# Performance work log

Measured on AMD Instinct MI355X. Metric: run time of the kernel, lower is better.

The kernel has to match this reference:

```python
import jax, jax.numpy as jnp
import numpy as np

BN_EPS = 1e-5

@jax.custom_vjp
def ste_sign(x):
    return jnp.sign(x)

def _ste_fwd(x):
    return jnp.sign(x), x

def _ste_bwd(x, g):
    # straight-through estimator with hardtanh clipping
    return (g * (jnp.abs(x) <= 1.0).astype(g.dtype),)

ste_sign.defvjp(_ste_fwd, _ste_bwd)

def bi_conv_bn_relu(h, W, scale, gamma, beta):
    # h: [B, Cin, K, N]; W: [Cout, Cin] (1x1 conv); scale/gamma/beta: [Cout]
    ba = ste_sign(h)                      # binarize activations
    bw = ste_sign(W)                      # binarize weights
    y = jnp.einsum('oi,bikn->bokn', bw, ba) * scale[None, :, None, None]
    # BatchNorm2d, training-mode batch statistics over (B, K, N)
    mean = jnp.mean(y, axis=(0, 2, 3), keepdims=True)
    var = jnp.var(y, axis=(0, 2, 3), keepdims=True)
    y = gamma[None, :, None, None] * (y - mean) * jax.lax.rsqrt(var + BN_EPS) + beta[None, :, None, None]
    return jax.nn.relu(y)

def setup_inputs() -> dict:
    key = jax.random.key(0)
    sizes = [64, 64, 64, 128]
    B, N, K = 8, 1024, 32
    ks = jax.random.split(key, 16)
    inp = {"agg_feat": jax.random.normal(ks[0], (B * N, K, sizes[0]), dtype=jnp.float32)}
    j = 1
    for i in range(1, len(sizes)):
        cin, cout = sizes[i - 1], sizes[i]
        inp[f"W{i}"] = jax.random.normal(ks[j], (cout, cin), dtype=jnp.float32) * 0.1; j += 1
        inp[f"s{i}"] = jax.random.uniform(ks[j], (cout,), dtype=jnp.float32, minval=0.05, maxval=0.2); j += 1
        inp[f"g{i}"] = jnp.ones((cout,), dtype=jnp.float32)
        inp[f"b{i}"] = jnp.zeros((cout,), dtype=jnp.float32)
    return inp

def reference(agg_feat, W1, s1, g1, b1, W2, s2, g2, b2, W3, s3, g3, b3):
    B = 8
    M, K, D = agg_feat.shape
    # view(B, -1, K, D).permute(0, 3, 2, 1) -> [B, D, K, N]
    h = agg_feat.reshape(B, M // B, K, D).transpose(0, 3, 2, 1)
    h = bi_conv_bn_relu(h, W1, s1, g1, b1)
    h = bi_conv_bn_relu(h, W2, s2, g2, b2)
    h = bi_conv_bn_relu(h, W3, s3, g3, b3)
    h = jnp.max(h, axis=2)                 # max-pool over neighbors -> [B, C, N]
    C = h.shape[1]
    return h.transpose(0, 2, 1).reshape(-1, C)  # [B*N, C]
```

## Files before the change

### kernel.cpp

```cpp
#include <hip/hip_runtime.h>


typedef unsigned long long u64;

#define P_TOTAL (8192 * 32)
#define NREP 16

__device__ __forceinline__ u64 bcast64(u64 x, int p) {
    unsigned lo = __builtin_amdgcn_readlane((unsigned)x, p);
    unsigned hi = __builtin_amdgcn_readlane((unsigned)(x >> 32), p);
    return ((u64)hi << 32) | lo;
}

__device__ __forceinline__ u64 pack_stats(int sd, int sq) {
    return ((u64)(unsigned)sd << 32) | (u64)(unsigned)sq;
}

__device__ __forceinline__ void affine_from_stats(const u64* __restrict__ st,
        int c, const float* __restrict__ scale, const float* __restrict__ gamma,
        const float* __restrict__ beta, int cparam, float& a, float& b) {
    u64 v = 0;
    #pragma unroll
    for (int r = 0; r < NREP; ++r) v += st[r * 256 + c];
    int sd = (int)(v >> 32);
    int sq = (int)(unsigned)(v & 0xFFFFFFFFull);
    const double invN = 1.0 / (double)P_TOTAL;
    double m = (double)sd * invN;
    double var = (double)sq * invN - m * m;
    double sc = (double)scale[cparam];
    double inv = 1.0 / sqrt(sc * sc * var + 1e-5);
    double g = (double)gamma[cparam];
    a = (float)(g * inv * sc);
    b = (float)((double)beta[cparam] - g * inv * sc * m);
}

__device__ __forceinline__ int make_thresh(float a, float b, bool& flip) {
    if (a == 0.f) { flip = false; return (b > 0.f) ? -65 : 65; }
    double r = -(double)b / (double)a;
    r = fmin(fmax(r, -1e6), 1e6);
    int t0 = (int)floor(r);
    int T;
    if (a > 0.f) {
        flip = false;
        T = t0 + 2;
        if (fmaf(a, (float)(t0 + 1), b) > 0.f) T = t0 + 1;
        if (fmaf(a, (float)(t0    ), b) > 0.f) T = t0;
        if (fmaf(a, (float)(t0 - 1), b) > 0.f) T = t0 - 1;
    } else {
        flip = true;
        int H = t0 - 2;
        if (fmaf(a, (float)(t0 - 1), b) > 0.f) H = t0 - 1;
        if (fmaf(a, (float)(t0    ), b) > 0.f) H = t0;
        if (fmaf(a, (float)(t0 + 1), b) > 0.f) H = t0 + 1;
        T = -H;
    }
    return max(-65, min(65, T));
}

__global__ void k0_pack(const float* __restrict__ W1, const float* __restrict__ W2,
                        const float* __restrict__ W3,
                        ulonglong2* __restrict__ wp1, ulonglong2* __restrict__ wp2,
                        ulonglong2* __restrict__ wp3, u64* __restrict__ stats) {
    int t = threadIdx.x;
    #pragma unroll
    for (int r = 0; r < NREP; ++r) stats[r * 256 + t] = 0;
    if (t < 64) {
        u64 s = 0, nz = 0;
        for (int c = 0; c < 64; ++c) {
            float w = W1[t * 64 + c];
            int p = ((c & 3) << 4) | (c >> 2);
            if (w > 0.f) s |= 1ull << p;
            if (w != 0.f) nz |= 1ull << p;
        }
        wp1[t] = make_ulonglong2(s, nz);
    } else if (t < 128) {
        int o = t - 64;
        u64 pos = 0, neg = 0;
        for (int c = 0; c < 64; ++c) {
            float w = W2[o * 64 + c];
            if (w > 0.f) pos |= 1ull << c;
            if (w < 0.f) neg |= 1ull << c;
        }
        wp2[o] = make_ulonglong2(pos, neg);
    } else {
        int o = t - 128;
        u64 pos = 0, neg = 0;
        for (int c = 0; c < 64; ++c) {
            float w = W3[o * 64 + c];
            if (w > 0.f) pos |= 1ull << c;
            if (w < 0.f) neg |= 1ull << c;
        }
        wp3[o] = make_ulonglong2(pos, neg);
    }
}

__global__ void __launch_bounds__(256) k1_pack_stats(
    const float4* __restrict__ in4, const ulonglong2* __restrict__ wp1,
    ulonglong2* __restrict__ A1, u64* __restrict__ stats) {
    const int lane = threadIdx.x & 63;
    const int wib = threadIdx.x >> 6;
    const int wid = (blockIdx.x << 2) | wib;
    const ulonglong2 w = wp1[lane];
    const int sh = (lane >> 4) << 4;
    const size_t base = (size_t)wid * 512 + lane;

    float4 v0 = in4[base];
    float4 v1 = in4[base + 64];
    float4 v2 = in4[base + 128];
    float4 v3 = in4[base + 192];
    float4 v4 = in4[base + 256];
    float4 v5 = in4[base + 320];
    float4 v6 = in4[base + 384];
    float4 v7 = in4[base + 448];

    int sd = 0, sq = 0;
    auto proc = [&](float4 v, int q0) {
        u64 bs0 = __ballot(v.x > 0.f), bn0 = __ballot(v.x != 0.f);
        u64 bs1 = __ballot(v.y > 0.f), bn1 = __ballot(v.y != 0.f);
        u64 bs2 = __ballot(v.z > 0.f), bn2 = __ballot(v.z != 0.f);
        u64 bs3 = __ballot(v.w > 0.f), bn3 = __ballot(v.w != 0.f);
        u64 myS = ((bs0 >> sh) & 0xFFFFull) | (((bs1 >> sh) & 0xFFFFull) << 16)
                | (((bs2 >> sh) & 0xFFFFull) << 32) | (((bs3 >> sh) & 0xFFFFull) << 48);
        u64 myN = ((bn0 >> sh) & 0xFFFFull) | (((bn1 >> sh) & 0xFFFFull) << 16)
                | (((bn2 >> sh) & 0xFFFFull) << 32) | (((bn3 >> sh) & 0xFFFFull) << 48);
        if ((lane & 15) == 0) A1[q0 + (lane >> 4)] = make_ulonglong2(myS, myN);
        #pragma unroll
        for (int p = 0; p < 4; ++p) {
            const int s2 = p << 4;
            u64 as = ((bs0 >> s2) & 0xFFFFull) | (((bs1 >> s2) & 0xFFFFull) << 16)
                   | (((bs2 >> s2) & 0xFFFFull) << 32) | (((bs3 >> s2) & 0xFFFFull) << 48);
            u64 an = ((bn0 >> s2) & 0xFFFFull) | (((bn1 >> s2) & 0xFFFFull) << 16)
                   | (((bn2 >> s2) & 0xFFFFull) << 32) | (((bn3 >> s2) & 0xFFFFull) << 48);
            u64 mnz = an & w.y;
            int dot = __popcll(mnz) - 2 * __popcll(mnz & (as ^ w.x));
            sd += dot; sq += dot * dot;
        }
    };
    const int q_base = wid * 32;
    proc(v0, q_base);      proc(v1, q_base + 4);
    proc(v2, q_base + 8);  proc(v3, q_base + 12);
    proc(v4, q_base + 16); proc(v5, q_base + 20);
    proc(v6, q_base + 24); proc(v7, q_base + 28);

    __shared__ int rd[4][64], rq[4][64];
    rd[wib][lane] = sd; rq[wib][lane] = sq;
    __syncthreads();
    if (threadIdx.x < 64) {
        int td = rd[0][lane] + rd[1][lane] + rd[2][lane] + rd[3][lane];
        int tq = rq[0][lane] + rq[1][lane] + rq[2][lane] + rq[3][lane];
        atomicAdd(&stats[(blockIdx.x & (NREP - 1)) * 256 + lane], pack_stats(td, tq));
    }
}

__global__ void __launch_bounds__(256, 4) k2_bin1_stats2(
    const ulonglong2* __restrict__ A1, const ulonglong2* __restrict__ wp1,
    const ulonglong2* __restrict__ wp2, const float* __restrict__ scale,
    const float* __restrict__ gamma, const float* __restrict__ beta,
    u64* __restrict__ A2, u64* __restrict__ stats) {
    const int lane = threadIdx.x & 63;
    const int wib = threadIdx.x >> 6;
    const int wid = (blockIdx.x << 2) | wib;
    float a, b;
    affine_from_stats(stats, lane, scale, gamma, beta, lane, a, b);
    bool flip;
    const int T = make_thresh(a, b, flip);
    ulonglong2 w1 = wp1[lane];
    const u64 w1S = flip ? ~w1.x : w1.x;
    const u64 w1N = w1.y;
    const ulonglong2 w2 = wp2[lane];

    const int q0 = wid * 64;
    const ulonglong2 aa = A1[q0 + lane];
    u64 mymask = 0;
    int sd = 0, sq = 0;
    #pragma unroll 8
    for (int p = 0; p < 64; ++p) {
        u64 as = bcast64(aa.x, p);
        u64 an = bcast64(aa.y, p);
        u64 mnz = an & w1N;
        int dot1 = __popcll(mnz) - 2 * __popcll(mnz & (as ^ w1S));
        u64 A = __ballot(dot1 >= T);
        mymask = (lane == p) ? A : mymask;
        int d2 = __popcll(A & w2.x) - __popcll(A & w2.y);
        sd += d2; sq += d2 * d2;
    }
    A2[q0 + lane] = mymask;

    __shared__ int rd[4][64], rq[4][64];
    rd[wib][lane] = sd; rq[wib][lane] = sq;
    __syncthreads();
    if (threadIdx.x < 64) {
        int td = rd[0][lane] + rd[1][lane] + rd[2][lane] + rd[3][lane];
        int tq = rq[0][lane] + rq[1][lane] + rq[2][lane] + rq[3][lane];
        atomicAdd(&stats[(blockIdx.x & (NREP - 1)) * 256 + 64 + lane], pack_stats(td, tq));
    }
}

__global__ void __launch_bounds__(256, 4) k3_bin2_stats3(
    const u64* __restrict__ A2, const ulonglong2* __restrict__ wp2,
    const ulonglong2* __restrict__ wp3, const float* __restrict__ scale,
    const float* __restrict__ gamma, const float* __restrict__ beta,
    short* __restrict__ dmm, u64* __restrict__ stats) {
    const int lane = threadIdx.x & 63;
    const int wib = threadIdx.x >> 6;
    const int wid = (blockIdx.x << 2) | wib;
    float a, b;
    affine_from_stats(stats, 64 + lane, scale, gamma, beta, lane, a, b);
    bool flip;
    const int T = make_thresh(a, b, flip);
    const ulonglong2 w2 = wp2[lane];
    const u64 w2P = flip ? w2.y : w2.x;
    const u64 w2N = flip ? w2.x : w2.y;
    const ulonglong2 w3a = wp3[lane];
    const ulonglong2 w3b = wp3[lane + 64];

    const int q0 = wid * 64;
    const u64 aa = A2[q0 + lane];
    int sda = 0, sqa = 0, sdb = 0, sqb = 0;
    #pragma unroll
    for (int r = 0; r < 2; ++r) {
        int maxa = -127, mina = 127, maxb = -127, minb = 127;
        #pragma unroll 8
        for (int pp = 0; pp < 32; ++pp) {
            const int p = (r << 5) | pp;
            u64 A = bcast64(aa, p);
            int d2 = __popcll(A & w2P) - __popcll(A & w2N);
            u64 A3 = __ballot(d2 >= T);
            int da = __popcll(A3 & w3a.x) - __popcll(A3 & w3a.y);
            int db = __popcll(A3 & w3b.x) - __popcll(A3 & w3b.y);
            sda += da; sqa += da * da; sdb += db; sqb += db * db;
            maxa = max(maxa, da); mina = min(mina, da);
            maxb = max(maxb, db); minb = min(minb, db);
        }
        const int m = (q0 >> 5) + r;
        dmm[m * 128 + lane]      = (short)((maxa & 0xFF) | ((mina & 0xFF) << 8));
        dmm[m * 128 + 64 + lane] = (short)((maxb & 0xFF) | ((minb & 0xFF) << 8));
    }
    __shared__ int rda[4][64], rqa[4][64], rdb[4][64], rqb[4][64];
    rda[wib][lane] = sda; rqa[wib][lane] = sqa;
    rdb[wib][lane] = sdb; rqb[wib][lane] = sqb;
    __syncthreads();
    if (threadIdx.x < 64) {
        const int rep = (blockIdx.x & (NREP - 1)) * 256;
        int tda = rda[0][lane] + rda[1][lane] + rda[2][lane] + rda[3][lane];
        int tqa = rqa[0][lane] + rqa[1][lane] + rqa[2][lane] + rqa[3][lane];
        int tdb = rdb[0][lane] + rdb[1][lane] + rdb[2][lane] + rdb[3][lane];
        int tqb = rqb[0][lane] + rqb[1][lane] + rqb[2][lane] + rqb[3][lane];
        atomicAdd(&stats[rep + 128 + lane], pack_stats(tda, tqa));
        atomicAdd(&stats[rep + 192 + lane], pack_stats(tdb, tqb));
    }
}

__global__ void __launch_bounds__(256) k4_out(
    const short* __restrict__ dmm, const float* __restrict__ scale,
    const float* __restrict__ gamma, const float* __restrict__ beta,
    const u64* __restrict__ stats, float* __restrict__ out) {
    __shared__ float sa[128], sb[128];
    if (threadIdx.x < 128)
        affine_from_stats(stats, 128 + threadIdx.x, scale, gamma, beta,
                          threadIdx.x, sa[threadIdx.x], sb[threadIdx.x]);
    __syncthreads();
    const int idx = blockIdx.x * 256 + threadIdx.x;
    const int o = idx & 127;
    short pk = dmm[idx];
    int mx = (signed char)(pk & 0xFF);
    int mn = (signed char)((pk >> 8) & 0xFF);
    float a = sa[o], b = sb[o];
    float v = fmaf(a, (float)(a >= 0.f ? mx : mn), b);
    out[idx] = fmaxf(v, 0.f);
}

extern "C" void kernel_launch(void* const* d_in, const int* in_sizes, int n_in,
                              void* d_out, int out_size, void* d_ws, size_t ws_size,
                              hipStream_t stream) {
    const float* agg = (const float*)d_in[0];
    const float* W1 = (const float*)d_in[1];
    const float* s1 = (const float*)d_in[2];
    const float* g1 = (const float*)d_in[3];
    const float* b1 = (const float*)d_in[4];
    const float* W2 = (const float*)d_in[5];
    const float* s2 = (const float*)d_in[6];
    const float* g2 = (const float*)d_in[7];
    const float* b2 = (const float*)d_in[8];
    const float* W3 = (const float*)d_in[9];
    const float* s3 = (const float*)d_in[10];
    const float* g3 = (const float*)d_in[11];
    const float* b3 = (const float*)d_in[12];
    float* out = (float*)d_out;

    char* ws = (char*)d_ws;
    ulonglong2* wp1 = (ulonglong2*)(ws + 0);
    ulonglong2* wp2 = (ulonglong2*)(ws + 1024);
    ulonglong2* wp3 = (ulonglong2*)(ws + 2048);
    u64* stats = (u64*)(ws + 4096);
    ulonglong2* A1 = (ulonglong2*)(ws + 65536);
    u64* A2 = (u64*)(ws + 65536 + (size_t)P_TOTAL * 16);
    short* dmm = (short*)(ws + 65536 + (size_t)P_TOTAL * 24);

    k0_pack<<<1, 256, 0, stream>>>(W1, W2, W3, wp1, wp2, wp3, stats);
    k1_pack_stats<<<2048, 256, 0, stream>>>((const float4*)agg, wp1, A1, stats);
    k2_bin1_stats2<<<1024, 256, 0, stream>>>(A1, wp1, wp2, s1, g1, b1, A2, stats);
    k3_bin2_stats3<<<1024, 256, 0, stream>>>(A2, wp2, wp3, s2, g2, b2, dmm, stats);
    k4_out<<<4096, 256, 0, stream>>>(dmm, s3, g3, b3, stats, out);
}
```

Before: 74.30 us.

## Halve per-wave work in bin kernels, share thresholds per block, vectorize weight pack

The binarized layer-2 and layer-3 kernels now have each wave handle 32 points instead of 64, with twice as many blocks launched, which doubles parallelism and shortens the serial readlane/ballot loop. Thresholds derived from batch statistics are computed once per block by 64 threads and shared through LDS, instead of being recomputed by every wave. The weight-packing kernel reads rows with float4 loads, and the output kernel uses 512-thread blocks. The occupancy hint in launch_bounds is dropped, and the extra block-level synchronization and doubled atomic traffic on the stats slots add some overhead.

```diff
diff --git a/kernel.cpp b/kernel.cpp
--- a/kernel.cpp
+++ b/kernel.cpp
@@ -2,6 +2,7 @@
 
 
 typedef unsigned long long u64;
+typedef unsigned int u32;
 
 #define P_TOTAL (8192 * 32)
 #define NREP 16
@@ -57,41 +58,57 @@
     return max(-65, min(65, T));
 }
 
-__global__ void k0_pack(const float* __restrict__ W1, const float* __restrict__ W2,
-                        const float* __restrict__ W3,
-                        ulonglong2* __restrict__ wp1, ulonglong2* __restrict__ wp2,
-                        ulonglong2* __restrict__ wp3, u64* __restrict__ stats) {
-    int t = threadIdx.x;
+__device__ __forceinline__ void block_params(const u64* __restrict__ stats,
+        int stat_off, const float* __restrict__ scale, const float* __restrict__ gamma,
+        const float* __restrict__ beta, int* gT, int* gF) {
+    const int t = threadIdx.x;
+    if (t < 64) {
+        float a, b;
+        affine_from_stats(stats, stat_off + t, scale, gamma, beta, t, a, b);
+        bool flip;
+        gT[t] = make_thresh(a, b, flip);
+        gF[t] = flip ? 1 : 0;
+    }
+    __syncthreads();
+}
+
+__global__ void __launch_bounds__(256) k0_pack(
+    const float* __restrict__ W1, const float* __restrict__ W2,
+    const float* __restrict__ W3, ulonglong2* __restrict__ wp1,
+    ulonglong2* __restrict__ wp2, ulonglong2* __restrict__ wp3,
+    u64* __restrict__ stats) {
+    const int t = threadIdx.x;
     #pragma unroll
     for (int r = 0; r < NREP; ++r) stats[r * 256 + t] = 0;
-    if (t < 64) {
-        u64 s = 0, nz = 0;
-        for (int c = 0; c < 64; ++c) {
-            float w = W1[t * 64 + c];
-            int p = ((c & 3) << 4) | (c >> 2);
-            if (w > 0.f) s |= 1ull << p;
-            if (w != 0.f) nz |= 1ull << p;
+
+    const float* src;
+    ulonglong2* dst;
+    bool perm, l1;
+    if (t < 64)       { src = W1 + t * 64;         dst = wp1 + t;         perm = true;  l1 = true;  }
+    else if (t < 128) { src = W2 + (t - 64) * 64;  dst = wp2 + (t - 64);  perm = false; l1 = false; }
+    else              { src = W3 + (t - 128) * 64; dst = wp3 + (t - 128); perm = false; l1 = false; }
+
+    const float4* s4 = (const float4*)src;
+    float4 v[16];
+    #pragma unroll
+    for (int j = 0; j < 16; ++j) v[j] = s4[j];
+
+    u64 hiM = 0, loM = 0;
+    #pragma unroll
+    for (int j = 0; j < 16; ++j) {
+        const float e0 = v[j].x, e1 = v[j].y, e2 = v[j].z, e3 = v[j].w;
+        #pragma unroll
+        for (int k = 0; k < 4; ++k) {
+            const float w = (k == 0) ? e0 : (k == 1) ? e1 : (k == 2) ? e2 : e3;
+            const int c = 4 * j + k;
+            const int p = perm ? (((c & 3) << 4) | (c >> 2)) : c;
+            const bool bh = (w > 0.f);
+            const bool bl = l1 ? (w != 0.f) : (w < 0.f);
+            if (bh) hiM |= 1ull << p;
+            if (bl) loM |= 1ull << p;
         }
-        wp1[t] = make_ulonglong2(s, nz);
-    } else if (t < 128) {
-        int o = t - 64;
-        u64 pos = 0, neg = 0;
-        for (int c = 0; c < 64; ++c) {
-            float w = W2[o * 64 + c];
-            if (w > 0.f) pos |= 1ull << c;
-            if (w < 0.f) neg |= 1ull << c;
-        }
-        wp2[o] = make_ulonglong2(pos, neg);
-    } else {
-        int o = t - 128;
-        u64 pos = 0, neg = 0;
-        for (int c = 0; c < 64; ++c) {
-            float w = W3[o * 64 + c];
-            if (w > 0.f) pos |= 1ull << c;
-            if (w < 0.f) neg |= 1ull << c;
-        }
-        wp3[o] = make_ulonglong2(pos, neg);
-    }
+    }
+    *dst = make_ulonglong2(hiM, loM);
 }
 
 __global__ void __launch_bounds__(256) k1_pack_stats(
@@ -152,39 +169,39 @@
     }
 }
 
-__global__ void __launch_bounds__(256, 4) k2_bin1_stats2(
+__global__ void __launch_bounds__(256) k2_bin1_stats2(
     const ulonglong2* __restrict__ A1, const ulonglong2* __restrict__ wp1,
     const ulonglong2* __restrict__ wp2, const float* __restrict__ scale,
     const float* __restrict__ gamma, const float* __restrict__ beta,
     u64* __restrict__ A2, u64* __restrict__ stats) {
+    __shared__ int gT[64], gF[64];
+    block_params(stats, 0, scale, gamma, beta, gT, gF);
+
     const int lane = threadIdx.x & 63;
     const int wib = threadIdx.x >> 6;
     const int wid = (blockIdx.x << 2) | wib;
-    float a, b;
-    affine_from_stats(stats, lane, scale, gamma, beta, lane, a, b);
-    bool flip;
-    const int T = make_thresh(a, b, flip);
+    const int T = gT[lane];
+    const bool flip = gF[lane] != 0;
     ulonglong2 w1 = wp1[lane];
     const u64 w1S = flip ? ~w1.x : w1.x;
     const u64 w1N = w1.y;
     const ulonglong2 w2 = wp2[lane];
 
-    const int q0 = wid * 64;
-    const ulonglong2 aa = A1[q0 + lane];
+    const u64 av = ((const u64*)A1)[(size_t)wid * 64 + lane];
     u64 mymask = 0;
     int sd = 0, sq = 0;
     #pragma unroll 8
-    for (int p = 0; p < 64; ++p) {
-        u64 as = bcast64(aa.x, p);
-        u64 an = bcast64(aa.y, p);
+    for (int p = 0; p < 32; ++p) {
+        u64 as = bcast64(av, 2 * p);
+        u64 an = bcast64(av, 2 * p + 1);
         u64 mnz = an & w1N;
         int dot1 = __popcll(mnz) - 2 * __popcll(mnz & (as ^ w1S));
         u64 A = __ballot(dot1 >= T);
-        mymask = (lane == p) ? A : mymask;
+        if (lane == p) mymask = A;
         int d2 = __popcll(A & w2.x) - __popcll(A & w2.y);
         sd += d2; sq += d2 * d2;
     }
-    A2[q0 + lane] = mymask;
+    if (lane < 32) A2[(size_t)wid * 32 + lane] = mymask;
 
     __shared__ int rd[4][64], rq[4][64];
     rd[wib][lane] = sd; rq[wib][lane] = sq;
@@ -196,46 +213,44 @@
     }
 }
 
-__global__ void __launch_bounds__(256, 4) k3_bin2_stats3(
+__global__ void __launch_bounds__(256) k3_bin2_stats3(
     const u64* __restrict__ A2, const ulonglong2* __restrict__ wp2,
     const ulonglong2* __restrict__ wp3, const float* __restrict__ scale,
     const float* __restrict__ gamma, const float* __restrict__ beta,
     short* __restrict__ dmm, u64* __restrict__ stats) {
+    __shared__ int gT[64], gF[64];
+    block_params(stats, 64, scale, gamma, beta, gT, gF);
+
     const int lane = threadIdx.x & 63;
     const int wib = threadIdx.x >> 6;
     const int wid = (blockIdx.x << 2) | wib;
-    float a, b;
-    affine_from_stats(stats, 64 + lane, scale, gamma, beta, lane, a, b);
-    bool flip;
-    const int T = make_thresh(a, b, flip);
+    const int T = gT[lane];
+    const bool flip = gF[lane] != 0;
     const ulonglong2 w2 = wp2[lane];
     const u64 w2P = flip ? w2.y : w2.x;
     const u64 w2N = flip ? w2.x : w2.y;
     const ulonglong2 w3a = wp3[lane];
     const ulonglong2 w3b = wp3[lane + 64];
 
-    const int q0 = wid * 64;
-    const u64 aa = A2[q0 + lane];
+    const u32 a32 = ((const u32*)A2)[(size_t)wid * 64 + lane];
     int sda = 0, sqa = 0, sdb = 0, sqb = 0;
-    #pragma unroll
-    for (int r = 0; r < 2; ++r) {
-        int maxa = -127, mina = 127, maxb = -127, minb = 127;
-        #pragma unroll 8
-        for (int pp = 0; pp < 32; ++pp) {
-            const int p = (r << 5) | pp;
-            u64 A = bcast64(aa, p);
-            int d2 = __popcll(A & w2P) - __popcll(A & w2N);
-            u64 A3 = __ballot(d2 >= T);
-            int da = __popcll(A3 & w3a.x) - __popcll(A3 & w3a.y);
-            int db = __popcll(A3 & w3b.x) - __popcll(A3 & w3b.y);
-            sda += da; sqa += da * da; sdb += db; sqb += db * db;
-            maxa = max(maxa, da); mina = min(mina, da);
-            maxb = max(maxb, db); minb = min(minb, db);
-        }
-        const int m = (q0 >> 5) + r;
-        dmm[m * 128 + lane]      = (short)((maxa & 0xFF) | ((mina & 0xFF) << 8));
-        dmm[m * 128 + 64 + lane] = (short)((maxb & 0xFF) | ((minb & 0xFF) << 8));
-    }
+    int maxa = -127, mina = 127, maxb = -127, minb = 127;
+    #pragma unroll 8
+    for (int p = 0; p < 32; ++p) {
+        u32 lo = __builtin_amdgcn_readlane(a32, 2 * p);
+        u32 hi = __builtin_amdgcn_readlane(a32, 2 * p + 1);
+        u64 A = ((u64)hi << 32) | lo;
+        int d2 = __popcll(A & w2P) - __popcll(A & w2N);
+        u64 A3 = __ballot(d2 >= T);
+        int da = __popcll(A3 & w3a.x) - __popcll(A3 & w3a.y);
+        int db = __popcll(A3 & w3b.x) - __popcll(A3 & w3b.y);
+        sda += da; sqa += da * da; sdb += db; sqb += db * db;
+        maxa = max(maxa, da); mina = min(mina, da);
+        maxb = max(maxb, db); minb = min(minb, db);
+    }
+    dmm[wid * 128 + lane]      = (short)((maxa & 0xFF) | ((mina & 0xFF) << 8));
+    dmm[wid * 128 + 64 + lane] = (short)((maxb & 0xFF) | ((minb & 0xFF) << 8));
+
     __shared__ int rda[4][64], rqa[4][64], rdb[4][64], rqb[4][64];
     rda[wib][lane] = sda; rqa[wib][lane] = sqa;
     rdb[wib][lane] = sdb; rqb[wib][lane] = sqb;
@@ -251,7 +266,7 @@
     }
 }
 
-__global__ void __launch_bounds__(256) k4_out(
+__global__ void __launch_bounds__(512) k4_out(
     const short* __restrict__ dmm, const float* __restrict__ scale,
     const float* __restrict__ gamma, const float* __restrict__ beta,
     const u64* __restrict__ stats, float* __restrict__ out) {
@@ -260,7 +275,7 @@
         affine_from_stats(stats, 128 + threadIdx.x, scale, gamma, beta,
                           threadIdx.x, sa[threadIdx.x], sb[threadIdx.x]);
     __syncthreads();
-    const int idx = blockIdx.x * 256 + threadIdx.x;
+    const int idx = blockIdx.x * 512 + threadIdx.x;
     const int o = idx & 127;
     short pk = dmm[idx];
     int mx = (signed char)(pk & 0xFF);
@@ -299,7 +314,7 @@
 
     k0_pack<<<1, 256, 0, stream>>>(W1, W2, W3, wp1, wp2, wp3, stats);
     k1_pack_stats<<<2048, 256, 0, stream>>>((const float4*)agg, wp1, A1, stats);
-    k2_bin1_stats2<<<1024, 256, 0, stream>>>(A1, wp1, wp2, s1, g1, b1, A2, stats);
-    k3_bin2_stats3<<<1024, 256, 0, stream>>>(A2, wp2, wp3, s2, g2, b2, dmm, stats);
-    k4_out<<<4096, 256, 0, stream>>>(dmm, s3, g3, b3, stats, out);
-}
+    k2_bin1_stats2<<<2048, 256, 0, stream>>>(A1, wp1, wp2, s1, g1, b1, A2, stats);
+    k3_bin2_stats3<<<2048, 256, 0, stream>>>(A2, wp2, wp3, s2, g2, b2, dmm, stats);
+    k4_out<<<2048, 512, 0, stream>>>(dmm, s3, g3, b3, stats, out);
+}
```

Result: faster. 72.18 us (-2.9%).

## Replace popcount binary dot products with int8 MFMA matrix ops

Applied to the files above, without the earlier changes.

Layers 1-3 now store activations as int8 sign values (+1/-1/0) and compute the binary 1x1 convolutions with 16x16x64 int8 MFMA instead of per-lane popcount loops driven by readlane broadcasts. Thresholded results are re-packed into bitmasks via ballot, then expanded back into MFMA fragments through a shared-memory lookup table and ds_bpermute. The layer-1 intermediate grows from 2 bits to 8 bits per channel, which adds memory traffic. The final kernel now uses 512-thread blocks.

```diff
diff --git a/kernel.cpp b/kernel.cpp
--- a/kernel.cpp
+++ b/kernel.cpp
@@ -2,18 +2,35 @@
 
 
 typedef unsigned long long u64;
+typedef unsigned int u32;
+typedef int v4i __attribute__((ext_vector_type(4)));
 
 #define P_TOTAL (8192 * 32)
 #define NREP 16
 
-__device__ __forceinline__ u64 bcast64(u64 x, int p) {
-    unsigned lo = __builtin_amdgcn_readlane((unsigned)x, p);
-    unsigned hi = __builtin_amdgcn_readlane((unsigned)(x >> 32), p);
-    return ((u64)hi << 32) | lo;
-}
-
 __device__ __forceinline__ u64 pack_stats(int sd, int sq) {
     return ((u64)(unsigned)sd << 32) | (u64)(unsigned)sq;
+}
+
+__device__ __forceinline__ v4i mfma_i8(v4i a, v4i b, v4i c) {
+    return __builtin_amdgcn_mfma_i32_16x16x64_i8(a, b, c, 0, 0, 0);
+}
+
+__device__ __forceinline__ v4i pack_wfrag(const float* __restrict__ W, int g, int lane) {
+    const float* p = W + (g * 16 + (lane & 15)) * 64 + (lane >> 4) * 16;
+    v4i r;
+    #pragma unroll
+    for (int d = 0; d < 4; ++d) {
+        u32 w = 0;
+        #pragma unroll
+        for (int b = 0; b < 4; ++b) {
+            float x = p[d * 4 + b];
+            u32 s = (x > 0.f) ? 1u : ((x < 0.f) ? 0xFFu : 0u);
+            w |= s << (8 * b);
+        }
+        r[d] = (int)w;
+    }
+    return r;
 }
 
 __device__ __forceinline__ void affine_from_stats(const u64* __restrict__ st,
@@ -57,51 +74,74 @@
     return max(-65, min(65, T));
 }
 
-__global__ void k0_pack(const float* __restrict__ W1, const float* __restrict__ W2,
-                        const float* __restrict__ W3,
-                        ulonglong2* __restrict__ wp1, ulonglong2* __restrict__ wp2,
-                        ulonglong2* __restrict__ wp3, u64* __restrict__ stats) {
-    int t = threadIdx.x;
+__device__ __forceinline__ void build_lut(u64* lut) {
+    if (threadIdx.x < 256) {
+        int t = threadIdx.x;
+        u64 e = 0;
+        #pragma unroll
+        for (int i = 0; i < 8; ++i) e |= (u64)((t >> i) & 1) << (8 * i);
+        lut[t] = e;
+    }
+}
+
+__device__ __forceinline__ v4i frag_from_vst(u32 vst, const u64* lut, int lane) {
+    int src = 8 * (((lane >> 4) << 2) | (lane & 3));
+    u32 lo = (u32)__builtin_amdgcn_ds_bpermute(src, (int)vst);
+    u32 hi = (u32)__builtin_amdgcn_ds_bpermute(src + 4, (int)vst);
+    u64 bits = ((u64)hi << 32) | lo;
+    u32 b16 = (u32)(bits >> ((((lane & 15) >> 2)) * 16)) & 0xFFFFu;
+    u64 e0 = lut[b16 & 0xFF], e1 = lut[b16 >> 8];
+    v4i a;
+    a[0] = (int)(u32)e0; a[1] = (int)(u32)(e0 >> 32);
+    a[2] = (int)(u32)e1; a[3] = (int)(u32)(e1 >> 32);
+    return a;
+}
+
+__device__ __forceinline__ v4i frag_from_bits(u64 bits, const u64* lut, int lane) {
+    u32 b16 = (u32)(bits >> ((((lane & 15) >> 2)) * 16)) & 0xFFFFu;
+    u64 e0 = lut[b16 & 0xFF], e1 = lut[b16 >> 8];
+    v4i a;
+    a[0] = (int)(u32)e0; a[1] = (int)(u32)(e0 >> 32);
+    a[2] = (int)(u32)e1; a[3] = (int)(u32)(e1 >> 32);
+    return a;
+}
+
+__device__ __forceinline__ u32 vst_select(u32 vst, u64 m, int pi, int lane) {
+    u32 sel = (lane & 1) ? (u32)(m >> 32) : (u32)m;
+    return ((lane >> 1) == pi) ? sel : vst;
+}
+
+__global__ void k0_pack(const float* __restrict__ W1, ulonglong2* __restrict__ wp1,
+                        u64* __restrict__ stats) {
+    const int t = threadIdx.x;
     #pragma unroll
     for (int r = 0; r < NREP; ++r) stats[r * 256 + t] = 0;
     if (t < 64) {
+        const float4* s4 = (const float4*)(W1 + t * 64);
         u64 s = 0, nz = 0;
-        for (int c = 0; c < 64; ++c) {
-            float w = W1[t * 64 + c];
-            int p = ((c & 3) << 4) | (c >> 2);
-            if (w > 0.f) s |= 1ull << p;
-            if (w != 0.f) nz |= 1ull << p;
+        #pragma unroll
+        for (int j = 0; j < 16; ++j) {
+            float4 v = s4[j];
+            #pragma unroll
+            for (int k = 0; k < 4; ++k) {
+                const float w = (k == 0) ? v.x : (k == 1) ? v.y : (k == 2) ? v.z : v.w;
+                const int c = 4 * j + k;
+                const int p = ((c & 3) << 4) | (c >> 2);
+                if (w > 0.f) s |= 1ull << p;
+                if (w != 0.f) nz |= 1ull << p;
+            }
         }
         wp1[t] = make_ulonglong2(s, nz);
-    } else if (t < 128) {
-        int o = t - 64;
-        u64 pos = 0, neg = 0;
-        for (int c = 0; c < 64; ++c) {
-            float w = W2[o * 64 + c];
-            if (w > 0.f) pos |= 1ull << c;
-            if (w < 0.f) neg |= 1ull << c;
-        }
-        wp2[o] = make_ulonglong2(pos, neg);
-    } else {
-        int o = t - 128;
-        u64 pos = 0, neg = 0;
-        for (int c = 0; c < 64; ++c) {
-            float w = W3[o * 64 + c];
-            if (w > 0.f) pos |= 1ull << c;
-            if (w < 0.f) neg |= 1ull << c;
-        }
-        wp3[o] = make_ulonglong2(pos, neg);
-    }
-}
-
-__global__ void __launch_bounds__(256) k1_pack_stats(
+    }
+}
+
+__global__ void __launch_bounds__(256) kA(
     const float4* __restrict__ in4, const ulonglong2* __restrict__ wp1,
-    ulonglong2* __restrict__ A1, u64* __restrict__ stats) {
+    u32* __restrict__ A1u, u64* __restrict__ stats) {
     const int lane = threadIdx.x & 63;
     const int wib = threadIdx.x >> 6;
     const int wid = (blockIdx.x << 2) | wib;
     const ulonglong2 w = wp1[lane];
-    const int sh = (lane >> 4) << 4;
     const size_t base = (size_t)wid * 512 + lane;
 
     float4 v0 = in4[base];
@@ -114,16 +154,14 @@
     float4 v7 = in4[base + 448];
 
     int sd = 0, sq = 0;
-    auto proc = [&](float4 v, int q0) {
+    auto sgn = [](float x) -> u32 { return x > 0.f ? 1u : (x < 0.f ? 0xFFu : 0u); };
+    auto proc = [&](float4 v, int j) {
+        u32 pk = sgn(v.x) | (sgn(v.y) << 8) | (sgn(v.z) << 16) | (sgn(v.w) << 24);
+        A1u[base + (size_t)j * 64] = pk;
         u64 bs0 = __ballot(v.x > 0.f), bn0 = __ballot(v.x != 0.f);
         u64 bs1 = __ballot(v.y > 0.f), bn1 = __ballot(v.y != 0.f);
         u64 bs2 = __ballot(v.z > 0.f), bn2 = __ballot(v.z != 0.f);
         u64 bs3 = __ballot(v.w > 0.f), bn3 = __ballot(v.w != 0.f);
-        u64 myS = ((bs0 >> sh) & 0xFFFFull) | (((bs1 >> sh) & 0xFFFFull) << 16)
-                | (((bs2 >> sh) & 0xFFFFull) << 32) | (((bs3 >> sh) & 0xFFFFull) << 48);
-        u64 myN = ((bn0 >> sh) & 0xFFFFull) | (((bn1 >> sh) & 0xFFFFull) << 16)
-                | (((bn2 >> sh) & 0xFFFFull) << 32) | (((bn3 >> sh) & 0xFFFFull) << 48);
-        if ((lane & 15) == 0) A1[q0 + (lane >> 4)] = make_ulonglong2(myS, myN);
         #pragma unroll
         for (int p = 0; p < 4; ++p) {
             const int s2 = p << 4;
@@ -136,11 +174,8 @@
             sd += dot; sq += dot * dot;
         }
     };
-    const int q_base = wid * 32;
-    proc(v0, q_base);      proc(v1, q_base + 4);
-    proc(v2, q_base + 8);  proc(v3, q_base + 12);
-    proc(v4, q_base + 16); proc(v5, q_base + 20);
-    proc(v6, q_base + 24); proc(v7, q_base + 28);
+    proc(v0, 0); proc(v1, 1); proc(v2, 2); proc(v3, 3);
+    proc(v4, 4); proc(v5, 5); proc(v6, 6); proc(v7, 7);
 
     __shared__ int rd[4][64], rq[4][64];
     rd[wib][lane] = sd; rq[wib][lane] = sq;
@@ -152,106 +187,180 @@
     }
 }
 
-__global__ void __launch_bounds__(256, 4) k2_bin1_stats2(
-    const ulonglong2* __restrict__ A1, const ulonglong2* __restrict__ wp1,
-    const ulonglong2* __restrict__ wp2, const float* __restrict__ scale,
-    const float* __restrict__ gamma, const float* __restrict__ beta,
-    u64* __restrict__ A2, u64* __restrict__ stats) {
+__global__ void __launch_bounds__(256) kC(
+    const v4i* __restrict__ A1f, const float* __restrict__ W1,
+    const float* __restrict__ W2, const float* __restrict__ s1,
+    const float* __restrict__ g1, const float* __restrict__ b1,
+    u32* __restrict__ A2B, u64* __restrict__ stats) {
+    __shared__ u64 lut[256];
+    __shared__ int Tl[64], Fl[64];
+    __shared__ u64 red[4][4][64];
+    build_lut(lut);
+    if (threadIdx.x < 64) {
+        float a, b;
+        affine_from_stats(stats, threadIdx.x, s1, g1, b1, threadIdx.x, a, b);
+        bool fl;
+        Tl[threadIdx.x] = make_thresh(a, b, fl);
+        Fl[threadIdx.x] = fl ? 1 : 0;
+    }
+    __syncthreads();
+
     const int lane = threadIdx.x & 63;
     const int wib = threadIdx.x >> 6;
-    const int wid = (blockIdx.x << 2) | wib;
-    float a, b;
-    affine_from_stats(stats, lane, scale, gamma, beta, lane, a, b);
-    bool flip;
-    const int T = make_thresh(a, b, flip);
-    ulonglong2 w1 = wp1[lane];
-    const u64 w1S = flip ? ~w1.x : w1.x;
-    const u64 w1N = w1.y;
-    const ulonglong2 w2 = wp2[lane];
-
-    const int q0 = wid * 64;
-    const ulonglong2 aa = A1[q0 + lane];
-    u64 mymask = 0;
-    int sd = 0, sq = 0;
-    #pragma unroll 8
-    for (int p = 0; p < 64; ++p) {
-        u64 as = bcast64(aa.x, p);
-        u64 an = bcast64(aa.y, p);
-        u64 mnz = an & w1N;
-        int dot1 = __popcll(mnz) - 2 * __popcll(mnz & (as ^ w1S));
-        u64 A = __ballot(dot1 >= T);
-        mymask = (lane == p) ? A : mymask;
-        int d2 = __popcll(A & w2.x) - __popcll(A & w2.y);
-        sd += d2; sq += d2 * d2;
-    }
-    A2[q0 + lane] = mymask;
-
-    __shared__ int rd[4][64], rq[4][64];
-    rd[wib][lane] = sd; rq[wib][lane] = sq;
+    const int wg = (blockIdx.x << 2) | wib;
+
+    v4i B1[4], B2[4];
+    int T1[4], F1[4];
+    #pragma unroll
+    for (int g = 0; g < 4; ++g) {
+        B1[g] = pack_wfrag(W1, g, lane);
+        B2[g] = pack_wfrag(W2, g, lane);
+        T1[g] = Tl[g * 16 + (lane & 15)];
+        F1[g] = Fl[g * 16 + (lane & 15)];
+    }
+
+    u64 st2[4] = {0, 0, 0, 0};
+    const v4i zero = {0, 0, 0, 0};
+    #pragma unroll
+    for (int t = 0; t < 4; ++t) {
+        const int tile = wg * 4 + t;
+        const int tb = tile * 16;
+        v4i a1 = A1f[(size_t)(tb + (lane & 15)) * 4 + (lane >> 4)];
+        u32 vst = 0;
+        #pragma unroll
+        for (int g = 0; g < 4; ++g) {
+            v4i d = mfma_i8(a1, B1[g], zero);
+            #pragma unroll
+            for (int r = 0; r < 4; ++r) {
+                int dd = F1[g] ? -d[r] : d[r];
+                u64 m = __ballot(dd >= T1[g]);
+                vst = vst_select(vst, m, g * 4 + r, lane);
+            }
+        }
+        if (lane < 32) A2B[(size_t)tile * 32 + lane] = vst;
+        v4i a2 = frag_from_vst(vst, lut, lane);
+        #pragma unroll
+        for (int g = 0; g < 4; ++g) {
+            v4i d2 = mfma_i8(a2, B2[g], zero);
+            #pragma unroll
+            for (int r = 0; r < 4; ++r) {
+                int v = d2[r];
+                st2[g] += ((u64)(u32)v << 32) | (u32)(v * v);
+            }
+        }
+    }
+    #pragma unroll
+    for (int g = 0; g < 4; ++g) red[wib][g][lane] = st2[g];
     __syncthreads();
     if (threadIdx.x < 64) {
-        int td = rd[0][lane] + rd[1][lane] + rd[2][lane] + rd[3][lane];
-        int tq = rq[0][lane] + rq[1][lane] + rq[2][lane] + rq[3][lane];
-        atomicAdd(&stats[(blockIdx.x & (NREP - 1)) * 256 + 64 + lane], pack_stats(td, tq));
-    }
-}
-
-__global__ void __launch_bounds__(256, 4) k3_bin2_stats3(
-    const u64* __restrict__ A2, const ulonglong2* __restrict__ wp2,
-    const ulonglong2* __restrict__ wp3, const float* __restrict__ scale,
-    const float* __restrict__ gamma, const float* __restrict__ beta,
+        const int g = threadIdx.x >> 4, c = threadIdx.x & 15;
+        u64 tot = 0;
+        #pragma unroll
+        for (int w = 0; w < 4; ++w)
+            #pragma unroll
+            for (int lg = 0; lg < 4; ++lg) tot += red[w][g][c + 16 * lg];
+        atomicAdd(&stats[(blockIdx.x & (NREP - 1)) * 256 + 64 + threadIdx.x], tot);
+    }
+}
+
+__global__ void __launch_bounds__(256) kD(
+    const u64* __restrict__ A2B64, const float* __restrict__ W2,
+    const float* __restrict__ W3, const float* __restrict__ s2,
+    const float* __restrict__ g2, const float* __restrict__ b2,
     short* __restrict__ dmm, u64* __restrict__ stats) {
+    __shared__ u64 lut[256];
+    __shared__ int Tl[64], Fl[64];
+    __shared__ u64 red[4][8][64];
+    build_lut(lut);
+    if (threadIdx.x < 64) {
+        float a, b;
+        affine_from_stats(stats, 64 + threadIdx.x, s2, g2, b2, threadIdx.x, a, b);
+        bool fl;
+        Tl[threadIdx.x] = make_thresh(a, b, fl);
+        Fl[threadIdx.x] = fl ? 1 : 0;
+    }
+    __syncthreads();
+
     const int lane = threadIdx.x & 63;
     const int wib = threadIdx.x >> 6;
-    const int wid = (blockIdx.x << 2) | wib;
-    float a, b;
-    affine_from_stats(stats, 64 + lane, scale, gamma, beta, lane, a, b);
-    bool flip;
-    const int T = make_thresh(a, b, flip);
-    const ulonglong2 w2 = wp2[lane];
-    const u64 w2P = flip ? w2.y : w2.x;
-    const u64 w2N = flip ? w2.x : w2.y;
-    const ulonglong2 w3a = wp3[lane];
-    const ulonglong2 w3b = wp3[lane + 64];
-
-    const int q0 = wid * 64;
-    const u64 aa = A2[q0 + lane];
-    int sda = 0, sqa = 0, sdb = 0, sqb = 0;
-    #pragma unroll
-    for (int r = 0; r < 2; ++r) {
-        int maxa = -127, mina = 127, maxb = -127, minb = 127;
-        #pragma unroll 8
-        for (int pp = 0; pp < 32; ++pp) {
-            const int p = (r << 5) | pp;
-            u64 A = bcast64(aa, p);
-            int d2 = __popcll(A & w2P) - __popcll(A & w2N);
-            u64 A3 = __ballot(d2 >= T);
-            int da = __popcll(A3 & w3a.x) - __popcll(A3 & w3a.y);
-            int db = __popcll(A3 & w3b.x) - __popcll(A3 & w3b.y);
-            sda += da; sqa += da * da; sdb += db; sqb += db * db;
-            maxa = max(maxa, da); mina = min(mina, da);
-            maxb = max(maxb, db); minb = min(minb, db);
-        }
-        const int m = (q0 >> 5) + r;
-        dmm[m * 128 + lane]      = (short)((maxa & 0xFF) | ((mina & 0xFF) << 8));
-        dmm[m * 128 + 64 + lane] = (short)((maxb & 0xFF) | ((minb & 0xFF) << 8));
-    }
-    __shared__ int rda[4][64], rqa[4][64], rdb[4][64], rqb[4][64];
-    rda[wib][lane] = sda; rqa[wib][lane] = sqa;
-    rdb[wib][lane] = sdb; rqb[wib][lane] = sqb;
-    __syncthreads();
-    if (threadIdx.x < 64) {
-        const int rep = (blockIdx.x & (NREP - 1)) * 256;
-        int tda = rda[0][lane] + rda[1][lane] + rda[2][lane] + rda[3][lane];
-        int tqa = rqa[0][lane] + rqa[1][lane] + rqa[2][lane] + rqa[3][lane];
-        int tdb = rdb[0][lane] + rdb[1][lane] + rdb[2][lane] + rdb[3][lane];
-        int tqb = rqb[0][lane] + rqb[1][lane] + rqb[2][lane] + rqb[3][lane];
-        atomicAdd(&stats[rep + 128 + lane], pack_stats(tda, tqa));
-        atomicAdd(&stats[rep + 192 + lane], pack_stats(tdb, tqb));
-    }
-}
-
-__global__ void __launch_bounds__(256) k4_out(
+    const int wg = (blockIdx.x << 2) | wib;
+
+    v4i B2f[4], B3[8];
+    int T2[4], F2[4];
+    #pragma unroll
+    for (int g = 0; g < 4; ++g) {
+        B2f[g] = pack_wfrag(W2, g, lane);
+        T2[g] = Tl[g * 16 + (lane & 15)];
+        F2[g] = Fl[g * 16 + (lane & 15)];
+    }
+    #pragma unroll
+    for (int g = 0; g < 8; ++g) B3[g] = pack_wfrag(W3, g, lane);
+
+    u64 st3[8] = {0, 0, 0, 0, 0, 0, 0, 0};
+    const v4i zero = {0, 0, 0, 0};
+    const int bsrc = ((lane >> 4) << 2) | (lane & 3);
+    #pragma unroll
+    for (int rr = 0; rr < 2; ++rr) {
+        int mx[8], mn[8];
+        #pragma unroll
+        for (int g = 0; g < 8; ++g) { mx[g] = -127; mn[g] = 127; }
+        #pragma unroll
+        for (int tt = 0; tt < 2; ++tt) {
+            const int tile = wg * 4 + rr * 2 + tt;
+            u64 bits = A2B64[(size_t)tile * 16 + bsrc];
+            v4i a2 = frag_from_bits(bits, lut, lane);
+            u32 vst = 0;
+            #pragma unroll
+            for (int g = 0; g < 4; ++g) {
+                v4i d2 = mfma_i8(a2, B2f[g], zero);
+                #pragma unroll
+                for (int r = 0; r < 4; ++r) {
+                    int dd = F2[g] ? -d2[r] : d2[r];
+                    u64 m = __ballot(dd >= T2[g]);
+                    vst = vst_select(vst, m, g * 4 + r, lane);
+                }
+            }
+            v4i a3 = frag_from_vst(vst, lut, lane);
+            #pragma unroll
+            for (int g = 0; g < 8; ++g) {
+                v4i d3 = mfma_i8(a3, B3[g], zero);
+                #pragma unroll
+                for (int r = 0; r < 4; ++r) {
+                    int v = d3[r];
+                    st3[g] += ((u64)(u32)v << 32) | (u32)(v * v);
+                    mx[g] = max(mx[g], v);
+                    mn[g] = min(mn[g], v);
+                }
+            }
+        }
+        const int row = 2 * wg + rr;
+        #pragma unroll
+        for (int g = 0; g < 8; ++g) {
+            int x = mx[g];
+            x = max(x, __shfl_xor(x, 16));
+            x = max(x, __shfl_xor(x, 32));
+            int n = mn[g];
+            n = min(n, __shfl_xor(n, 16));
+            n = min(n, __shfl_xor(n, 32));
+            if (lane < 16)
+                dmm[row * 128 + g * 16 + lane] = (short)((x & 0xFF) | ((n & 0xFF) << 8));
+        }
+    }
+    #pragma unroll
+    for (int g = 0; g < 8; ++g) red[wib][g][lane] = st3[g];
+    __syncthreads();
+    if (threadIdx.x < 128) {
+        const int g = threadIdx.x >> 4, c = threadIdx.x & 15;
+        u64 tot = 0;
+        #pragma unroll
+        for (int w = 0; w < 4; ++w)
+            #pragma unroll
+            for (int lg = 0; lg < 4; ++lg) tot += red[w][g][c + 16 * lg];
+        atomicAdd(&stats[(blockIdx.x & (NREP - 1)) * 256 + 128 + threadIdx.x], tot);
+    }
+}
+
+__global__ void __launch_bounds__(512) kE(
     const short* __restrict__ dmm, const float* __restrict__ scale,
     const float* __restrict__ gamma, const float* __restrict__ beta,
     const u64* __restrict__ stats, float* __restrict__ out) {
@@ -260,7 +369,7 @@
         affine_from_stats(stats, 128 + threadIdx.x, scale, gamma, beta,
                           threadIdx.x, sa[threadIdx.x], sb[threadIdx.x]);
     __syncthreads();
-    const int idx = blockIdx.x * 256 + threadIdx.x;
+    const int idx = blockIdx.x * 512 + threadIdx.x;
     const int o = idx & 127;
     short pk = dmm[idx];
     int mx = (signed char)(pk & 0xFF);
@@ -290,16 +399,14 @@
 
     char* ws = (char*)d_ws;
     ulonglong2* wp1 = (ulonglong2*)(ws + 0);
-    ulonglong2* wp2 = (ulonglong2*)(ws + 1024);
-    ulonglong2* wp3 = (ulonglong2*)(ws + 2048);
     u64* stats = (u64*)(ws + 4096);
-    ulonglong2* A1 = (ulonglong2*)(ws + 65536);
-    u64* A2 = (u64*)(ws + 65536 + (size_t)P_TOTAL * 16);
-    short* dmm = (short*)(ws + 65536 + (size_t)P_TOTAL * 24);
-
-    k0_pack<<<1, 256, 0, stream>>>(W1, W2, W3, wp1, wp2, wp3, stats);
-    k1_pack_stats<<<2048, 256, 0, stream>>>((const float4*)agg, wp1, A1, stats);
-    k2_bin1_stats2<<<1024, 256, 0, stream>>>(A1, wp1, wp2, s1, g1, b1, A2, stats);
-    k3_bin2_stats3<<<1024, 256, 0, stream>>>(A2, wp2, wp3, s2, g2, b2, dmm, stats);
-    k4_out<<<4096, 256, 0, stream>>>(dmm, s3, g3, b3, stats, out);
-}
+    u32* A1u = (u32*)(ws + 65536);
+    u32* A2B = (u32*)(ws + 65536 + (size_t)16 * 1024 * 1024);
+    short* dmm = (short*)(ws + 65536 + (size_t)18 * 1024 * 1024);
+
+    k0_pack<<<1, 256, 0, stream>>>(W1, wp1, stats);
+    kA<<<2048, 256, 0, stream>>>((const float4*)agg, wp1, A1u, stats);
+    kC<<<1024, 256, 0, stream>>>((const v4i*)A1u, W1, W2, s1, g1, b1, A2B, stats);
+    kD<<<1024, 256, 0, stream>>>((const u64*)A2B, W2, W3, s2, g2, b2, dmm, stats);
+    kE<<<2048, 512, 0, stream>>>(dmm, s3, g3, b3, stats, out);
+}
```

New measurement: 94.19 us. 1.27x slower.
